# Kernel tuning notes

Hardware: AMD Instinct MI355X
Metric: run time of the kernel (lower is better)

The kernel has to match this reference:

```python
import jax, jax.numpy as jnp
import numpy as np

B, C, H, W, HEADS, S = 8, 512, 32, 32, 8, 77
CH = C // HEADS  # per-head channels = 64
GROUPS = 32      # GroupNorm32


def setup_inputs() -> dict:
    key = jax.random.key(0)
    ks = jax.random.split(key, 6)
    s = 0.02
    return {
        "x": jax.random.normal(ks[0], (B, C, H, W), jnp.float32),
        "encoder_out": jax.random.normal(ks[1], (B, C, S), jnp.float32),
        "capt_attn_mask": jax.random.bernoulli(ks[2], 0.9, (B, S)),
        "norm_scale": jnp.ones((C,), jnp.float32),
        "norm_bias": jnp.zeros((C,), jnp.float32),
        "qkv_w": jax.random.normal(ks[3], (3 * C, C), jnp.float32) * s,
        "qkv_b": jnp.zeros((3 * C,), jnp.float32),
        "ekv_w": jax.random.normal(ks[4], (2 * C, C), jnp.float32) * s,
        "ekv_b": jnp.zeros((2 * C,), jnp.float32),
        "proj_w": jax.random.normal(ks[5], (C, C), jnp.float32) * s,
        "proj_b": jnp.zeros((C,), jnp.float32),
    }


def reference(x, encoder_out, capt_attn_mask, norm_scale, norm_bias,
              qkv_w, qkv_b, ekv_w, ekv_b, proj_w, proj_b):
    b, c, h, w = x.shape
    T = h * w
    xf = x.reshape(b, c, T)

    # GroupNorm(32) in fp32 (GroupNorm32), affine
    xg = xf.reshape(b, GROUPS, c // GROUPS, T).astype(jnp.float32)
    mu = xg.mean(axis=(2, 3), keepdims=True)
    var = xg.var(axis=(2, 3), keepdims=True)
    nrm = ((xg - mu) * jax.lax.rsqrt(var + 1e-5)).reshape(b, c, T)
    nrm = nrm * norm_scale[None, :, None] + norm_bias[None, :, None]

    # 1x1 conv1d qkv projection: [b, 3c, T]
    qkv = jnp.einsum('oc,bct->bot', qkv_w, nrm) + qkv_b[None, :, None]
    qkv = qkv.reshape(b * HEADS, 3 * CH, T)
    q, k, v = jnp.split(qkv, 3, axis=1)  # each [b*heads, CH, T]

    # encoder kv: [b, 2c, S] -> [b*heads, 2*CH, S]
    ekv = jnp.einsum('oc,bcs->bos', ekv_w, encoder_out) + ekv_b[None, :, None]
    ekv = ekv.reshape(b * HEADS, 2 * CH, S)
    ek, ev = jnp.split(ekv, 2, axis=1)
    k = jnp.concatenate([ek, k], axis=-1)  # [b*heads, CH, S+T]
    v = jnp.concatenate([ev, v], axis=-1)

    scale = 1.0 / np.sqrt(np.sqrt(CH))
    wgt = jnp.einsum('bct,bcs->bts', q * scale, k * scale).astype(jnp.float32)

    # additive mask; torch.tile over dim0 is head-major (row i -> batch i % b),
    # faithfully reproduced; self-attn part (last T cols) is all-visible.
    addm_capt = jnp.where(jnp.tile(capt_attn_mask, (HEADS, 1)), 0.0, -10000.0)
    addm = jnp.concatenate(
        [addm_capt, jnp.zeros((b * HEADS, T), jnp.float32)], axis=1)[:, None, :]
    wgt = jax.nn.softmax(wgt + addm, axis=-1).astype(v.dtype)

    out = jnp.einsum('bts,bcs->bct', wgt, v)  # [b*heads, CH, T]
    out = out.reshape(b, c, T)
    out = jnp.einsum('oc,bct->bot', proj_w, out) + proj_b[None, :, None]
    return (xf + out).reshape(b, c, h, w)
```

## Files before the change

### kernel.cpp

```cpp
#include <hip/hip_runtime.h>
#include <math.h>

#define BB 8
#define TT 1024
#define SS 77

typedef short v8s __attribute__((ext_vector_type(8)));
typedef float v4f __attribute__((ext_vector_type(4)));
typedef unsigned short u16x4 __attribute__((ext_vector_type(4)));
typedef unsigned short u16x8 __attribute__((ext_vector_type(8)));
typedef unsigned short u16;

#define SCALEF 0.424660891f
#define MASKNEG (-14426.95f)

__device__ __forceinline__ u16 f2bf(float f) {
  unsigned u = __float_as_uint(f);
  u = (u + 0x7fffu + ((u >> 16) & 1u)) >> 16;
  return (u16)u;
}
__device__ __forceinline__ u16 hi16(float f) {
  return (u16)(__float_as_uint(f) >> 16);
}
__device__ __forceinline__ float bf2f(u16 u) {
  return __uint_as_float(((unsigned)u) << 16);
}
__device__ __forceinline__ void gl_lds16(const void* g, void* l) {
  __builtin_amdgcn_global_load_lds(
      (const __attribute__((address_space(1))) void*)g,
      (__attribute__((address_space(3))) void*)l, 16, 0, 0);
}

__global__ __launch_bounds__(256) void prep_gn_kernel(
    const float* __restrict__ x, const float* __restrict__ scale,
    const float* __restrict__ bias, u16* __restrict__ nrmT,
    const float* __restrict__ qkv_w, const float* __restrict__ ekv_w,
    const float* __restrict__ proj_w, const float* __restrict__ enc,
    const float* __restrict__ qkv_b, const float* __restrict__ ekv_b,
    u16* __restrict__ wQK, u16* __restrict__ wV, u16* __restrict__ wEK,
    u16* __restrict__ wEV, u16* __restrict__ projwb, u16* __restrict__ encT,
    float* __restrict__ bQK, float* __restrict__ bV,
    float* __restrict__ bEK, float* __restrict__ bEV) {
  __shared__ u16 Xs[16 * 1024];
  __shared__ float red[8];
  int blk = blockIdx.x, tid = threadIdx.x;

  if (blk < 256) {
    int bg = blk;
    int b = bg >> 5, g = bg & 31;
    const float4* x4 = (const float4*)(x + (size_t)bg * 16384);
    float s = 0.f, sq = 0.f;
#pragma unroll
    for (int i = 0; i < 16; ++i) {
      int idx = tid + 256 * i;
      float4 v = x4[idx];
      s += v.x + v.y + v.z + v.w;
      sq += v.x * v.x + v.y * v.y + v.z * v.z + v.w * v.w;
      int c = idx >> 8, t4 = (idx & 255) * 4;
      u16x4 o; o.x = f2bf(v.x); o.y = f2bf(v.y); o.z = f2bf(v.z); o.w = f2bf(v.w);
      *(u16x4*)(Xs + c * 1024 + t4) = o;
    }
#pragma unroll
    for (int off = 32; off > 0; off >>= 1) {
      s += __shfl_down(s, off, 64);
      sq += __shfl_down(sq, off, 64);
    }
    int wave = tid >> 6;
    if ((tid & 63) == 0) { red[wave] = s; red[wave + 4] = sq; }
    __syncthreads();
    float ts = red[0] + red[1] + red[2] + red[3];
    float tq = red[4] + red[5] + red[6] + red[7];
    float mu = ts * (1.0f / 16384.0f);
    float var = tq * (1.0f / 16384.0f) - mu * mu;
    float rs = rsqrtf(var + 1e-5f);
    float scv[16], biv[16];
#pragma unroll
    for (int c = 0; c < 16; ++c) {
      float ss = scale[g * 16 + c] * rs;
      scv[c] = ss;
      biv[c] = bias[g * 16 + c] - mu * ss;
    }
#pragma unroll
    for (int j = 0; j < 4; ++j) {
      int t = tid + 256 * j;
      u16x8 o0, o1;
#pragma unroll
      for (int c = 0; c < 8; ++c)  o0[c] = f2bf(bf2f(Xs[c * 1024 + t]) * scv[c] + biv[c]);
#pragma unroll
      for (int c = 8; c < 16; ++c) o1[c - 8] = f2bf(bf2f(Xs[c * 1024 + t]) * scv[c] + biv[c]);
      u16* dst = nrmT + ((size_t)b * 1024 + t) * 512 + g * 16;
      *(u16x8*)dst = o0;
      *(u16x8*)(dst + 8) = o1;
    }
    return;
  }

  int p = blk - 256;
  if (p < 512) {
    int idx = p * 256 + tid;
    int n = idx >> 7, c4 = (idx & 127) * 4;
    int which = n >> 9, h = (n >> 6) & 7, ch = n & 63;
    int src = h * 192 + which * 64 + ch;
    float4 v = *(const float4*)(qkv_w + (size_t)src * 512 + c4);
    u16x4 o; o.x = f2bf(v.x * SCALEF); o.y = f2bf(v.y * SCALEF);
    o.z = f2bf(v.z * SCALEF); o.w = f2bf(v.w * SCALEF);
    *(u16x4*)(wQK + (size_t)n * 512 + c4) = o;
  } else if (p < 768) {
    int idx = (p - 512) * 256 + tid;
    int n = idx >> 7, c4 = (idx & 127) * 4;
    int h = n >> 6, ch = n & 63;
    int src = h * 192 + 128 + ch;
    float4 v = *(const float4*)(qkv_w + (size_t)src * 512 + c4);
    u16x4 o; o.x = f2bf(v.x); o.y = f2bf(v.y); o.z = f2bf(v.z); o.w = f2bf(v.w);
    *(u16x4*)(wV + (size_t)n * 512 + c4) = o;
  } else if (p < 1024) {
    int idx = (p - 768) * 256 + tid;
    int n = idx >> 7, c4 = (idx & 127) * 4;
    int h = n >> 6, ch = n & 63;
    int src = h * 128 + ch;
    float4 v = *(const float4*)(ekv_w + (size_t)src * 512 + c4);
    u16x4 o; o.x = f2bf(v.x * SCALEF); o.y = f2bf(v.y * SCALEF);
    o.z = f2bf(v.z * SCALEF); o.w = f2bf(v.w * SCALEF);
    *(u16x4*)(wEK + (size_t)n * 512 + c4) = o;
  } else if (p < 1280) {
    int idx = (p - 1024) * 256 + tid;
    int n = idx >> 7, c4 = (idx & 127) * 4;
    int h = n >> 6, ch = n & 63;
    int src = h * 128 + 64 + ch;
    float4 v = *(const float4*)(ekv_w + (size_t)src * 512 + c4);
    u16x4 o; o.x = f2bf(v.x); o.y = f2bf(v.y); o.z = f2bf(v.z); o.w = f2bf(v.w);
    *(u16x4*)(wEV + (size_t)n * 512 + c4) = o;
  } else if (p < 1536) {
    int idx = (p - 1280) * 256 + tid;
    float4 v = ((const float4*)proj_w)[idx];
    u16x4 o; o.x = f2bf(v.x); o.y = f2bf(v.y); o.z = f2bf(v.z); o.w = f2bf(v.w);
    *(u16x4*)(projwb + (size_t)idx * 4) = o;
  } else if (p < 2048) {
    int idx = (p - 1536) * 256 + tid;
    int b = idx >> 14, rem = idx & 16383;
    int s = rem >> 7, c = (rem & 127) * 4;
    u16x4 o; o.x = 0; o.y = 0; o.z = 0; o.w = 0;
    if (s < SS) {
      const float* pp = enc + ((size_t)b * 512 + c) * SS + s;
      o.x = f2bf(pp[0]); o.y = f2bf(pp[SS]); o.z = f2bf(pp[2 * SS]); o.w = f2bf(pp[3 * SS]);
    }
    *(u16x4*)(encT + ((size_t)b * 128 + s) * 512 + c) = o;
  } else {
    for (int i = tid; i < 2560; i += 256) {
      if (i < 1024) {
        int which = i >> 9, h = (i >> 6) & 7, ch = i & 63;
        bQK[i] = qkv_b[h * 192 + which * 64 + ch] * SCALEF;
      } else if (i < 1536) {
        int j = i - 1024; int h = j >> 6, ch = j & 63;
        bV[j] = qkv_b[h * 192 + 128 + ch];
      } else if (i < 2048) {
        int j = i - 1536; int h = j >> 6, ch = j & 63;
        bEK[j] = ekv_b[h * 128 + ch] * SCALEF;
      } else {
        int j = i - 2048; int h = j >> 6, ch = j & 63;
        bEV[j] = ekv_b[h * 128 + 64 + ch];
      }
    }
  }
}

__global__ __launch_bounds__(256) void proj_all(
    const u16* __restrict__ nrmT, const u16* __restrict__ encT,
    const u16* __restrict__ wQK, const u16* __restrict__ wEK,
    const u16* __restrict__ wV, const u16* __restrict__ wEV,
    const float* __restrict__ bQK, const float* __restrict__ bEK,
    const float* __restrict__ bV, const float* __restrict__ bEV,
    u16* __restrict__ Qh, u16* __restrict__ Kfull, u16* __restrict__ Vfull) {
  __shared__ __align__(16) u16 SH[16384];
  u16* As = SH;
  u16* Bs = SH + 8192;

  int job = blockIdx.x, bz = blockIdx.y;
  int tid = threadIdx.x;
  int lane = tid & 63, w = tid >> 6;
  int lan15 = lane & 15, quad = lane >> 4;
  int wm = w >> 1, wn = w & 1;

  int mode, m0, n0;
  const u16 *Ap, *Bp;
  const float* bias;
  u16 *dA = nullptr, *dB = nullptr;
  int TrA = 0, offA = 0, TrB = 0, offB = 0;
  int coff = 0;

  if (job < 64) {
    mode = 3; m0 = (job >> 3) * 128; n0 = (job & 7) * 128;
    Ap = nrmT + (size_t)bz * 1024 * 512; Bp = wQK; bias = bQK;
    dA = Qh; TrA = 1024; offA = 0; dB = Kfull; TrB = 1152; offB = 128;
  } else if (job < 68) {
    mode = 3; m0 = 0; n0 = (job - 64) * 128;
    Ap = encT + (size_t)bz * 128 * 512; Bp = wEK; bias = bEK;
    dA = Kfull; TrA = 1152; offA = 0; dB = Kfull; TrB = 1152; offB = 0;
  } else if (job < 100) {
    int jj = job - 68; mode = 0; m0 = (jj >> 3) * 128; n0 = (jj & 7) * 128;
    Ap = wV; Bp = nrmT + (size_t)bz * 1024 * 512; bias = bV;
    coff = 128;
  } else {
    int jj = job - 100; mode = 0; m0 = jj * 128; n0 = 0;
    Ap = wEV; Bp = encT + (size_t)bz * 128 * 512; bias = bEV;
    coff = 0;
  }

  int srow = lane >> 3;
  int schunk = (lane & 7) ^ srow;
  const char* Ag = (const char*)(Ap + (size_t)(m0 + w * 32 + srow) * 512) + schunk * 16;
  const char* Bg = (const char*)(Bp + (size_t)(n0 + w * 32 + srow) * 512) + schunk * 16;
  char* Al = (char*)As + w * 4096;
  char* Bl = (char*)Bs + w * 4096;

  v4f acc[4][4] = {};

  for (int step = 0; step < 8; ++step) {
    __syncthreads();
    int kb = step * 128;
#pragma unroll
    for (int i = 0; i < 4; ++i) gl_lds16(Ag + kb + i * 8192, Al + i * 1024);
#pragma unroll
    for (int i = 0; i < 4; ++i) gl_lds16(Bg + kb + i * 8192, Bl + i * 1024);
    __syncthreads();

#pragma unroll
    for (int ksub = 0; ksub < 2; ++ksub) {
      int ch = ((ksub * 4 + quad) ^ (lan15 & 7)) * 16;
      v8s a[4], bf[4];
#pragma unroll
      for (int i = 0; i < 4; ++i)
        a[i] = *(const v8s*)((const char*)As + (wm * 64 + i * 16 + lan15) * 128 + ch);
#pragma unroll
      for (int j = 0; j < 4; ++j)
        bf[j] = *(const v8s*)((const char*)Bs + (wn * 64 + j * 16 + lan15) * 128 + ch);
#pragma unroll
      for (int i = 0; i < 4; ++i)
#pragma unroll
        for (int j = 0; j < 4; ++j)
          acc[i][j] = __builtin_amdgcn_mfma_f32_16x16x32_bf16(a[i], bf[j], acc[i][j], 0, 0, 0);
    }
  }

  if (mode == 3) {
    u16* Tr = SH;
    for (int ph = 0; ph < 2; ++ph) {
      __syncthreads();
      if (wn == ph) {
#pragma unroll
        for (int j = 0; j < 4; ++j) {
          int n = n0 + wn * 64 + j * 16 + lan15;
          float bv_ = bias[n];
#pragma unroll
          for (int i = 0; i < 4; ++i)
#pragma unroll
            for (int r = 0; r < 4; ++r)
              Tr[(wm * 64 + i * 16 + quad * 4 + r) * 72 + j * 16 + lan15] =
                  f2bf(acc[i][j][r] + bv_);
        }
      }
      __syncthreads();
      int nb = n0 + ph * 64;
      u16* dst = (nb < 512) ? dA : dB;
      int Trows = (nb < 512) ? TrA : TrB;
      int roff  = (nb < 512) ? offA : offB;
      int hh = (nb & 511) >> 6;
      int row = tid >> 1, seg = (tid & 1) * 32;
      u16* dp = dst + ((size_t)(bz * 8 + hh) * Trows + roff + m0 + row) * 64 + seg;
#pragma unroll
      for (int g = 0; g < 4; ++g)
        *(u16x8*)(dp + g * 8) = *(const u16x8*)(Tr + row * 72 + seg + g * 8);
    }
  } else {
    u16* Tr = SH;
    u16* Cb = Vfull + (size_t)bz * 512 * 1152;
    for (int ph = 0; ph < 2; ++ph) {
      __syncthreads();
      if (wn == ph) {
#pragma unroll
        for (int i = 0; i < 4; ++i) {
          int ob = wm * 64 + i * 16 + quad * 4;
#pragma unroll
          for (int r = 0; r < 4; ++r) {
            float bi = bias[m0 + ob + r];
#pragma unroll
            for (int j = 0; j < 4; ++j)
              Tr[(ob + r) * 72 + j * 16 + lan15] = f2bf(acc[i][j][r] + bi);
          }
        }
      }
      __syncthreads();
      int row = tid >> 1, seg = (tid & 1) * 32;
      u16* dp = Cb + (size_t)(m0 + row) * 1152 + coff + n0 + ph * 64 + seg;
#pragma unroll
      for (int g = 0; g < 4; ++g)
        *(u16x8*)(dp + g * 8) = *(const u16x8*)(Tr + row * 72 + seg + g * 8);
    }
  }
}

__global__ __launch_bounds__(256) void proj_out(
    const u16* __restrict__ A, const u16* __restrict__ B,
    const float* __restrict__ bias, const float* __restrict__ res,
    float* __restrict__ Cf) {
  __shared__ __align__(16) u16 SH[16384];
  u16* As = SH;
  u16* Bs = SH + 8192;

  int tid = threadIdx.x;
  int lane = tid & 63, w = tid >> 6;
  int lan15 = lane & 15, quad = lane >> 4;
  int wm = w >> 1, wn = w & 1;
  int m0 = blockIdx.y * 128, n0 = blockIdx.x * 128;
  int bz = blockIdx.z;
  const u16* Bb = B + (size_t)bz * 1024 * 512;

  int srow = lane >> 3;
  int schunk = (lane & 7) ^ srow;
  const char* Ag = (const char*)(A + (size_t)(m0 + w * 32 + srow) * 512) + schunk * 16;
  const char* Bg = (const char*)(Bb + (size_t)(n0 + w * 32 + srow) * 512) + schunk * 16;
  char* Al = (char*)As + w * 4096;
  char* Bl = (char*)Bs + w * 4096;

  v4f acc[4][4] = {};

  for (int step = 0; step < 8; ++step) {
    __syncthreads();
    int kb = step * 128;
#pragma unroll
    for (int i = 0; i < 4; ++i) gl_lds16(Ag + kb + i * 8192, Al + i * 1024);
#pragma unroll
    for (int i = 0; i < 4; ++i) gl_lds16(Bg + kb + i * 8192, Bl + i * 1024);
    __syncthreads();

#pragma unroll
    for (int ksub = 0; ksub < 2; ++ksub) {
      int ch = ((ksub * 4 + quad) ^ (lan15 & 7)) * 16;
      v8s a[4], bf[4];
#pragma unroll
      for (int i = 0; i < 4; ++i)
        a[i] = *(const v8s*)((const char*)As + (wm * 64 + i * 16 + lan15) * 128 + ch);
#pragma unroll
      for (int j = 0; j < 4; ++j)
        bf[j] = *(const v8s*)((const char*)Bs + (wn * 64 + j * 16 + lan15) * 128 + ch);
#pragma unroll
      for (int i = 0; i < 4; ++i)
#pragma unroll
        for (int j = 0; j < 4; ++j)
          acc[i][j] = __builtin_amdgcn_mfma_f32_16x16x32_bf16(a[i], bf[j], acc[i][j], 0, 0, 0);
    }
  }

  const float* rb = res + (size_t)bz * 512 * 1024;
  float* Cb = Cf + (size_t)bz * 512 * 1024;
#pragma unroll
  for (int i = 0; i < 4; ++i) {
    int ob = m0 + wm * 64 + i * 16 + quad * 4;
#pragma unroll
    for (int r = 0; r < 4; ++r) {
      int o = ob + r;
      float bi = bias[o];
#pragma unroll
      for (int j = 0; j < 4; ++j) {
        int n = n0 + wn * 64 + j * 16 + lan15;
        Cb[(size_t)o * 1024 + n] = acc[i][j][r] + bi + rb[(size_t)o * 1024 + n];
      }
    }
  }
}

#define AOFF_K 0
#define AOFF_V 16384
#define AOFF_P 32768
#define AOFF_AM 51200
#define ASMEM  51712

__global__ __launch_bounds__(128, 2) void attn_kernel(
    const u16* __restrict__ Qh, const u16* __restrict__ Kf,
    const u16* __restrict__ Vf, const int* __restrict__ mask,
    u16* __restrict__ attnT) {
  __shared__ __align__(16) unsigned char smem[ASMEM];
  float* AM = (float*)(smem + AOFF_AM);

  int bh = blockIdx.x, b = bh >> 3, h = bh & 7;
  int t0 = blockIdx.y * 128;
  int tid = threadIdx.x;
  int lane = tid & 63, w = tid >> 6;
  int lan15 = lane & 15, quad = lane >> 4;
  int r8 = lane >> 3, c8 = lane & 7;
  int swE = (c8 ^ r8) * 8;

  const u16* Qb = Qh + (size_t)bh * 1024 * 64;
  const u16* Kb = Kf + (size_t)bh * 1152 * 64;
  const u16* Vb = Vf + (size_t)bh * 64 * 1152;
  char* Pw = (char*)smem + AOFF_P + w * 9216;
  u16* Pu = (u16*)Pw;

  AM[tid] = (tid < SS) ? ((mask[h * SS + tid] != 0) ? 0.f : MASKNEG) : -1e30f;

#pragma unroll
  for (int i = 0; i < 8; ++i)
    gl_lds16(Qb + (size_t)(t0 + w * 64 + i * 8 + r8) * 64 + swE, Pw + i * 1024);
#pragma unroll
  for (int i = 0; i < 4; ++i) {
    int row = w * 32 + i * 8;
    gl_lds16(Kb + (size_t)(row + r8) * 64 + swE, (char*)smem + AOFF_K + row * 128);
    gl_lds16(Vb + (size_t)(row + r8) * 1152 + swE, (char*)smem + AOFF_V + row * 128);
  }
  __syncthreads();

  v8s aq[4][2];
#pragma unroll
  for (int mt = 0; mt < 4; ++mt)
#pragma unroll
    for (int ks = 0; ks < 2; ++ks)
      aq[mt][ks] = *(const v8s*)(Pw + (mt * 16 + lan15) * 128 +
                                 (((ks * 4 + quad) ^ (lan15 & 7)) * 16));

  v4f O[4][4] = {};
  float lsum[4] = {};

  for (int c = 0; c < 18; ++c) {
    int cur = c & 1;
    if (c < 17) {
      int nb = cur ^ 1;
#pragma unroll
      for (int i = 0; i < 4; ++i) {
        int row = w * 32 + i * 8;
        gl_lds16(Kb + (size_t)((c + 1) * 64 + row + r8) * 64 + swE,
                 (char*)smem + AOFF_K + nb * 8192 + row * 128);
        gl_lds16(Vb + (size_t)(row + r8) * 1152 + (c + 1) * 64 + swE,
                 (char*)smem + AOFF_V + nb * 8192 + row * 128);
      }
    }
    const char* Kc = (const char*)smem + AOFF_K + cur * 8192;
    const char* Vc = (const char*)smem + AOFF_V + cur * 8192;

    v4f ST[4][4] = {};
#pragma unroll
    for (int ks = 0; ks < 2; ++ks) {
      int cofs = ((ks * 4 + quad) ^ (lan15 & 7)) * 16;
      v8s bk[4];
#pragma unroll
      for (int nt = 0; nt < 4; ++nt)
        bk[nt] = *(const v8s*)(Kc + (nt * 16 + lan15) * 128 + cofs);
#pragma unroll
      for (int nt = 0; nt < 4; ++nt)
#pragma unroll
        for (int mt = 0; mt < 4; ++mt)
          ST[nt][mt] = __builtin_amdgcn_mfma_f32_16x16x32_bf16(bk[nt], aq[mt][ks], ST[nt][mt], 0, 0, 0);
    }

    if (c < 2) {
#pragma unroll
      for (int nt = 0; nt < 4; ++nt)
#pragma unroll
        for (int r = 0; r < 4; ++r) {
          float a_ = AM[c * 64 + nt * 16 + quad * 4 + r];
#pragma unroll
          for (int mt = 0; mt < 4; ++mt) ST[nt][mt][r] += a_;
        }
    }

#pragma unroll
    for (int mt = 0; mt < 4; ++mt) {
#pragma unroll
      for (int nt = 0; nt < 4; ++nt) {
        float e0 = __builtin_amdgcn_exp2f(ST[nt][mt][0]);
        float e1 = __builtin_amdgcn_exp2f(ST[nt][mt][1]);
        float e2 = __builtin_amdgcn_exp2f(ST[nt][mt][2]);
        float e3 = __builtin_amdgcn_exp2f(ST[nt][mt][3]);
        u16x4 pk; pk.x = hi16(e0); pk.y = hi16(e1); pk.z = hi16(e2); pk.w = hi16(e3);
        *(u16x4*)&Pu[(mt * 16 + lan15) * 72 + nt * 16 + quad * 4] = pk;
        lsum[mt] += (e0 + e1) + (e2 + e3);
      }
    }

#pragma unroll
    for (int ks = 0; ks < 2; ++ks) {
      int cofs = ((ks * 4 + quad) ^ (lan15 & 7)) * 16;
      v8s ap[4], bv[4];
#pragma unroll
      for (int mt = 0; mt < 4; ++mt)
        ap[mt] = *(const v8s*)(Pw + (mt * 16 + lan15) * 144 + ks * 64 + quad * 16);
#pragma unroll
      for (int nc = 0; nc < 4; ++nc)
        bv[nc] = *(const v8s*)(Vc + (nc * 16 + lan15) * 128 + cofs);
#pragma unroll
      for (int nc = 0; nc < 4; ++nc)
#pragma unroll
        for (int mt = 0; mt < 4; ++mt)
          O[nc][mt] = __builtin_amdgcn_mfma_f32_16x16x32_bf16(bv[nc], ap[mt], O[nc][mt], 0, 0, 0);
    }
    __syncthreads();
  }

  float inv[4];
#pragma unroll
  for (int mt = 0; mt < 4; ++mt) {
    float v = lsum[mt];
    v += __shfl_xor(v, 16, 64);
    v += __shfl_xor(v, 32, 64);
    inv[mt] = 1.0f / v;
  }

#pragma unroll
  for (int mt = 0; mt < 4; ++mt) {
    int t = t0 + w * 64 + mt * 16 + lan15;
    u16* dp = attnT + ((size_t)b * 1024 + t) * 512 + h * 64 + quad * 4;
#pragma unroll
    for (int nc = 0; nc < 4; ++nc) {
      u16x4 pk;
      pk.x = f2bf(O[nc][mt][0] * inv[mt]);
      pk.y = f2bf(O[nc][mt][1] * inv[mt]);
      pk.z = f2bf(O[nc][mt][2] * inv[mt]);
      pk.w = f2bf(O[nc][mt][3] * inv[mt]);
      *(u16x4*)(dp + nc * 16) = pk;
    }
  }
}

extern "C" void kernel_launch(void* const* d_in, const int* in_sizes, int n_in,
                              void* d_out, int out_size, void* d_ws, size_t ws_size,
                              hipStream_t stream) {
  const float* x       = (const float*)d_in[0];
  const float* enc     = (const float*)d_in[1];
  const int*   mask    = (const int*)d_in[2];
  const float* nscale  = (const float*)d_in[3];
  const float* nbias   = (const float*)d_in[4];
  const float* qkv_w   = (const float*)d_in[5];
  const float* qkv_b   = (const float*)d_in[6];
  const float* ekv_w   = (const float*)d_in[7];
  const float* ekv_b   = (const float*)d_in[8];
  const float* proj_w  = (const float*)d_in[9];
  const float* proj_b  = (const float*)d_in[10];
  float* out = (float*)d_out;

  char* ws = (char*)d_ws;
  const size_t MiB = 1048576;
  u16* nrmT   = (u16*)(ws);
  u16* Qh     = (u16*)(ws + 8 * MiB);
  u16* Kfull  = (u16*)(ws + 16 * MiB);
  u16* Vfull  = (u16*)(ws + 26 * MiB);
  u16* attnT  = (u16*)(ws + 36 * MiB);
  u16* encT   = (u16*)(ws + 44 * MiB);
  u16* wQK    = (u16*)(ws + 45 * MiB);
  u16* wV     = (u16*)(ws + 46 * MiB);
  u16* wEK    = (u16*)(ws + 46 * MiB + 524288);
  u16* wEV    = (u16*)(ws + 47 * MiB);
  u16* projwb = (u16*)(ws + 47 * MiB + 524288);
  float* bQK  = (float*)(ws + 48 * MiB);
  float* bV   = (float*)(ws + 48 * MiB + 4096);
  float* bEK  = (float*)(ws + 48 * MiB + 6144);
  float* bEV  = (float*)(ws + 48 * MiB + 8192);

  prep_gn_kernel<<<dim3(2305), dim3(256), 0, stream>>>(
      x, nscale, nbias, nrmT, qkv_w, ekv_w, proj_w, enc, qkv_b, ekv_b,
      wQK, wV, wEK, wEV, projwb, encT, bQK, bV, bEK, bEV);

  proj_all<<<dim3(104, BB), dim3(256), 0, stream>>>(
      nrmT, encT, wQK, wEK, wV, wEV, bQK, bEK, bV, bEV, Qh, Kfull, Vfull);

  attn_kernel<<<dim3(64, 8), dim3(128), 0, stream>>>(
      Qh, Kfull, Vfull, mask, attnT);

  proj_out<<<dim3(8, 4, BB), dim3(256), 0, stream>>>(
      projwb, attnT, proj_b, x, out);
}
```

Baseline: 183.7 us.

## Split attention key dimension across warps with LDS atomic reduction

Result: slower. 269.7 us (+46.8%).

```diff
diff --git a/kernel.cpp b/kernel.cpp
--- a/kernel.cpp
+++ b/kernel.cpp
@@ -369,21 +369,26 @@
   }
 }
 
-#define AOFF_K 0
-#define AOFF_V 16384
-#define AOFF_P 32768
-#define AOFF_AM 51200
-#define ASMEM  51712
-
-__global__ __launch_bounds__(128, 2) void attn_kernel(
+#define KOFF 0
+#define VOFF 16384
+#define QOFF (VOFF + 16384)
+#define POFF 40960
+#define LOFF 61440
+#define IOFF 62464
+#define MOFF 62720
+#define ASMEM 63232
+
+__global__ __launch_bounds__(256) void attn_kernel(
     const u16* __restrict__ Qh, const u16* __restrict__ Kf,
     const u16* __restrict__ Vf, const int* __restrict__ mask,
     u16* __restrict__ attnT) {
   __shared__ __align__(16) unsigned char smem[ASMEM];
-  float* AM = (float*)(smem + AOFF_AM);
+  float* AM = (float*)(smem + MOFF);
+  float* Lw = (float*)(smem + LOFF);
+  float* AMinv = (float*)(smem + IOFF);
 
   int bh = blockIdx.x, b = bh >> 3, h = bh & 7;
-  int t0 = blockIdx.y * 128;
+  int t0 = blockIdx.y * 64;
   int tid = threadIdx.x;
   int lane = tid & 63, w = tid >> 6;
   int lan15 = lane & 15, quad = lane >> 4;
@@ -393,19 +398,17 @@
   const u16* Qb = Qh + (size_t)bh * 1024 * 64;
   const u16* Kb = Kf + (size_t)bh * 1152 * 64;
   const u16* Vb = Vf + (size_t)bh * 64 * 1152;
-  char* Pw = (char*)smem + AOFF_P + w * 9216;
-  u16* Pu = (u16*)Pw;
-
-  AM[tid] = (tid < SS) ? ((mask[h * SS + tid] != 0) ? 0.f : MASKNEG) : -1e30f;
-
-#pragma unroll
-  for (int i = 0; i < 8; ++i)
-    gl_lds16(Qb + (size_t)(t0 + w * 64 + i * 8 + r8) * 64 + swE, Pw + i * 1024);
-#pragma unroll
-  for (int i = 0; i < 4; ++i) {
-    int row = w * 32 + i * 8;
-    gl_lds16(Kb + (size_t)(row + r8) * 64 + swE, (char*)smem + AOFF_K + row * 128);
-    gl_lds16(Vb + (size_t)(row + r8) * 1152 + swE, (char*)smem + AOFF_V + row * 128);
+  char* Pw = (char*)smem + POFF + w * 5120;
+
+  if (tid < 128)
+    AM[tid] = (tid < SS) ? ((mask[h * SS + tid] != 0) ? 0.f : MASKNEG) : -1e30f;
+
+#pragma unroll
+  for (int i = 0; i < 2; ++i) {
+    int row = w * 16 + i * 8;
+    gl_lds16(Qb + (size_t)(t0 + row + r8) * 64 + swE, (char*)smem + QOFF + row * 128);
+    gl_lds16(Kb + (size_t)(row + r8) * 64 + swE, (char*)smem + KOFF + row * 128);
+    gl_lds16(Vb + (size_t)(row + r8) * 1152 + swE, (char*)smem + VOFF + row * 128);
   }
   __syncthreads();
 
@@ -414,109 +417,113 @@
   for (int mt = 0; mt < 4; ++mt)
 #pragma unroll
     for (int ks = 0; ks < 2; ++ks)
-      aq[mt][ks] = *(const v8s*)(Pw + (mt * 16 + lan15) * 128 +
+      aq[mt][ks] = *(const v8s*)((char*)smem + QOFF + (mt * 16 + lan15) * 128 +
                                  (((ks * 4 + quad) ^ (lan15 & 7)) * 16));
 
   v4f O[4][4] = {};
-  float lsum[4] = {};
+  float Lp[4] = {};
 
   for (int c = 0; c < 18; ++c) {
-    int cur = c & 1;
     if (c < 17) {
-      int nb = cur ^ 1;
-#pragma unroll
-      for (int i = 0; i < 4; ++i) {
-        int row = w * 32 + i * 8;
+      int kb = ((c + 1) & 1) * 8192;
+      int vb = ((c + 1) % 3) * 8192;
+#pragma unroll
+      for (int i = 0; i < 2; ++i) {
+        int row = w * 16 + i * 8;
         gl_lds16(Kb + (size_t)((c + 1) * 64 + row + r8) * 64 + swE,
-                 (char*)smem + AOFF_K + nb * 8192 + row * 128);
+                 (char*)smem + KOFF + kb + row * 128);
         gl_lds16(Vb + (size_t)(row + r8) * 1152 + (c + 1) * 64 + swE,
-                 (char*)smem + AOFF_V + nb * 8192 + row * 128);
+                 (char*)smem + VOFF + vb + row * 128);
       }
     }
-    const char* Kc = (const char*)smem + AOFF_K + cur * 8192;
-    const char* Vc = (const char*)smem + AOFF_V + cur * 8192;
-
-    v4f ST[4][4] = {};
+    const char* Kc = (const char*)smem + KOFF + (c & 1) * 8192;
+
+    v4f ST[4] = {};
 #pragma unroll
     for (int ks = 0; ks < 2; ++ks) {
       int cofs = ((ks * 4 + quad) ^ (lan15 & 7)) * 16;
-      v8s bk[4];
-#pragma unroll
-      for (int nt = 0; nt < 4; ++nt)
-        bk[nt] = *(const v8s*)(Kc + (nt * 16 + lan15) * 128 + cofs);
-#pragma unroll
-      for (int nt = 0; nt < 4; ++nt)
-#pragma unroll
-        for (int mt = 0; mt < 4; ++mt)
-          ST[nt][mt] = __builtin_amdgcn_mfma_f32_16x16x32_bf16(bk[nt], aq[mt][ks], ST[nt][mt], 0, 0, 0);
+      v8s bk = *(const v8s*)(Kc + (w * 16 + lan15) * 128 + cofs);
+#pragma unroll
+      for (int mt = 0; mt < 4; ++mt)
+        ST[mt] = __builtin_amdgcn_mfma_f32_16x16x32_bf16(bk, aq[mt][ks], ST[mt], 0, 0, 0);
     }
 
     if (c < 2) {
-#pragma unroll
-      for (int nt = 0; nt < 4; ++nt)
-#pragma unroll
-        for (int r = 0; r < 4; ++r) {
-          float a_ = AM[c * 64 + nt * 16 + quad * 4 + r];
-#pragma unroll
-          for (int mt = 0; mt < 4; ++mt) ST[nt][mt][r] += a_;
-        }
+      float am_[4];
+#pragma unroll
+      for (int r = 0; r < 4; ++r) am_[r] = AM[c * 64 + w * 16 + quad * 4 + r];
+#pragma unroll
+      for (int mt = 0; mt < 4; ++mt)
+#pragma unroll
+        for (int r = 0; r < 4; ++r) ST[mt][r] += am_[r];
     }
 
 #pragma unroll
     for (int mt = 0; mt < 4; ++mt) {
-#pragma unroll
-      for (int nt = 0; nt < 4; ++nt) {
-        float e0 = __builtin_amdgcn_exp2f(ST[nt][mt][0]);
-        float e1 = __builtin_amdgcn_exp2f(ST[nt][mt][1]);
-        float e2 = __builtin_amdgcn_exp2f(ST[nt][mt][2]);
-        float e3 = __builtin_amdgcn_exp2f(ST[nt][mt][3]);
-        u16x4 pk; pk.x = hi16(e0); pk.y = hi16(e1); pk.z = hi16(e2); pk.w = hi16(e3);
-        *(u16x4*)&Pu[(mt * 16 + lan15) * 72 + nt * 16 + quad * 4] = pk;
-        lsum[mt] += (e0 + e1) + (e2 + e3);
-      }
-    }
-
-#pragma unroll
-    for (int ks = 0; ks < 2; ++ks) {
-      int cofs = ((ks * 4 + quad) ^ (lan15 & 7)) * 16;
+      float e0 = __builtin_amdgcn_exp2f(ST[mt][0]);
+      float e1 = __builtin_amdgcn_exp2f(ST[mt][1]);
+      float e2 = __builtin_amdgcn_exp2f(ST[mt][2]);
+      float e3 = __builtin_amdgcn_exp2f(ST[mt][3]);
+      u16x4 pk; pk.x = hi16(e0); pk.y = hi16(e1); pk.z = hi16(e2); pk.w = hi16(e3);
+      *(u16x4*)(Pw + (mt * 16 + lan15) * 80 + (c & 1) * 32 + quad * 8) = pk;
+      Lp[mt] += (e0 + e1) + (e2 + e3);
+    }
+
+    if (c & 1) {
+      int vbE = ((c - 1) % 3) * 8192;
+      int vbO = (c % 3) * 8192;
+      int vsel = (quad < 2) ? vbE : vbO;
+      int cofsv = ((w * 2 + (quad & 1)) ^ (lan15 & 7)) * 16;
       v8s ap[4], bv[4];
 #pragma unroll
       for (int mt = 0; mt < 4; ++mt)
-        ap[mt] = *(const v8s*)(Pw + (mt * 16 + lan15) * 144 + ks * 64 + quad * 16);
+        ap[mt] = *(const v8s*)(Pw + (mt * 16 + lan15) * 80 + quad * 16);
 #pragma unroll
       for (int nc = 0; nc < 4; ++nc)
-        bv[nc] = *(const v8s*)(Vc + (nc * 16 + lan15) * 128 + cofs);
-#pragma unroll
-      for (int nc = 0; nc < 4; ++nc)
-#pragma unroll
-        for (int mt = 0; mt < 4; ++mt)
-          O[nc][mt] = __builtin_amdgcn_mfma_f32_16x16x32_bf16(bv[nc], ap[mt], O[nc][mt], 0, 0, 0);
+        bv[nc] = *(const v8s*)((char*)smem + VOFF + vsel + (nc * 16 + lan15) * 128 + cofsv);
+#pragma unroll
+      for (int mt = 0; mt < 4; ++mt)
+#pragma unroll
+        for (int nc = 0; nc < 4; ++nc)
+          O[mt][nc] = __builtin_amdgcn_mfma_f32_16x16x32_bf16(ap[mt], bv[nc], O[mt][nc], 0, 0, 0);
     }
     __syncthreads();
   }
 
-  float inv[4];
 #pragma unroll
   for (int mt = 0; mt < 4; ++mt) {
-    float v = lsum[mt];
+    float v = Lp[mt];
     v += __shfl_xor(v, 16, 64);
     v += __shfl_xor(v, 32, 64);
-    inv[mt] = 1.0f / v;
-  }
-
-#pragma unroll
-  for (int mt = 0; mt < 4; ++mt) {
-    int t = t0 + w * 64 + mt * 16 + lan15;
-    u16* dp = attnT + ((size_t)b * 1024 + t) * 512 + h * 64 + quad * 4;
-#pragma unroll
-    for (int nc = 0; nc < 4; ++nc) {
-      u16x4 pk;
-      pk.x = f2bf(O[nc][mt][0] * inv[mt]);
-      pk.y = f2bf(O[nc][mt][1] * inv[mt]);
-      pk.z = f2bf(O[nc][mt][2] * inv[mt]);
-      pk.w = f2bf(O[nc][mt][3] * inv[mt]);
-      *(u16x4*)(dp + nc * 16) = pk;
-    }
+    if (quad == 0) Lw[w * 64 + mt * 16 + lan15] = v;
+  }
+  float* Ot = (float*)(smem + VOFF);
+  for (int i = tid; i < 64 * 68; i += 256) Ot[i] = 0.f;
+  __syncthreads();
+
+#pragma unroll
+  for (int mt = 0; mt < 4; ++mt)
+#pragma unroll
+    for (int nc = 0; nc < 4; ++nc)
+#pragma unroll
+      for (int r = 0; r < 4; ++r)
+        atomicAdd(&Ot[(mt * 16 + quad * 4 + r) * 68 + nc * 16 + lan15], O[mt][nc][r]);
+  if (tid < 64)
+    AMinv[tid] = 1.0f / (Lw[tid] + Lw[64 + tid] + Lw[128 + tid] + Lw[192 + tid]);
+  __syncthreads();
+
+  {
+    int row = tid >> 2, seg = (tid & 3) * 16;
+    float inv = AMinv[row];
+    const float* src = Ot + row * 68 + seg;
+    u16x8 o0, o1;
+#pragma unroll
+    for (int k = 0; k < 8; ++k) o0[k] = f2bf(src[k] * inv);
+#pragma unroll
+    for (int k = 8; k < 16; ++k) o1[k - 8] = f2bf(src[k] * inv);
+    u16* dp = attnT + ((size_t)b * 1024 + t0 + row) * 512 + h * 64 + seg;
+    *(u16x8*)dp = o0;
+    *(u16x8*)(dp + 8) = o1;
   }
 }
 
@@ -561,7 +568,7 @@
   proj_all<<<dim3(104, BB), dim3(256), 0, stream>>>(
       nrmT, encT, wQK, wEK, wV, wEV, bQK, bEK, bV, bEV, Qh, Kfull, Vfull);
 
-  attn_kernel<<<dim3(64, 8), dim3(128), 0, stream>>>(
+  attn_kernel<<<dim3(64, 16), dim3(256), 0, stream>>>(
       Qh, Kfull, Vfull, mask, attnT);
 
   proj_out<<<dim3(8, 4, BB), dim3(256), 0, stream>>>(
```
